# Kernel optimization log

Hardware: AMD Instinct MI355X
Metric: run time of the kernel (lower is better)

Reference implementation:

```python
import jax, jax.numpy as jnp
import numpy as np

B, T, D, K = 16, 8192, 64, 1024


def setup_inputs() -> dict:
    key = jax.random.key(0)
    k1, k2 = jax.random.split(key)
    x = jax.random.normal(k1, (B, T, D, 1), dtype=jnp.float32)
    weight = jax.random.normal(k2, (K, D), dtype=jnp.float32)
    return {"x": x, "weight": weight}


def reference(x, weight):
    # x: [B, T, D, 1] -> squeeze trailing dim -> [B, T, D]
    xs = jnp.squeeze(x, axis=-1)
    x2 = jnp.sum(xs * xs, axis=-1, keepdims=True)          # [B, T, 1]
    e2 = jnp.sum(weight * weight, axis=-1)                 # [K]
    xe = jnp.einsum('btd,kd->btk', xs, weight)             # [B, T, K]
    dist2 = x2 - 2.0 * xe + e2                             # [B, T, K]
    indices = jnp.argmin(dist2, axis=-1)                   # [B, T] int
    quantized = jnp.take(weight, indices, axis=0)          # [B, T, D]
    return quantized, indices
```

## Files before the change

### kernel.cpp

```cpp
#include <hip/hip_runtime.h>

#define MTOK  131072
#define DIMD  64
#define KCODE 1024
#define TPB   128

typedef __bf16 bf16x8 __attribute__((ext_vector_type(8)));
typedef float  f32x4  __attribute__((ext_vector_type(4)));

__device__ __forceinline__ f32x4 mfma16(bf16x8 a, bf16x8 b, f32x4 c) {
    return __builtin_amdgcn_mfma_f32_16x16x32_bf16(a, b, c, 0, 0, 0);
}

__global__ __launch_bounds__(256) void prep_kernel(
    const float* __restrict__ w, __bf16* __restrict__ wpk,
    float* __restrict__ e2n, float* __restrict__ e2) {
    int cb  = blockIdx.x;
    int tid = threadIdx.x;
    int win = tid >> 6, lane = tid & 63;
    int q = lane >> 4, m = lane & 15;
    int k = cb * 16 + m;
    int d0 = (win & 1) * 32 + q * 8;
    const float* src = w + (size_t)k * DIMD + d0;
    float4 v0 = *(const float4*)(src);
    float4 v1 = *(const float4*)(src + 4);
    float f[8] = {v0.x, v0.y, v0.z, v0.w, v1.x, v1.y, v1.z, v1.w};
    bf16x8 o;
#pragma unroll
    for (int j = 0; j < 8; ++j) {
        __bf16 h = (__bf16)f[j];
        o[j] = (win < 2) ? h : (__bf16)(f[j] - (float)h);
    }
    *(bf16x8*)(wpk + ((size_t)(cb * 4 + win) * 64 + lane) * 8) = o;

    if (tid < 16) {
        int k2 = cb * 16 + tid;
        const float4* row = (const float4*)(w + (size_t)k2 * DIMD);
        float s = 0.f;
#pragma unroll
        for (int i = 0; i < 16; ++i) {
            float4 v = row[i];
            s = fmaf(v.x, v.x, s); s = fmaf(v.y, v.y, s);
            s = fmaf(v.z, v.z, s); s = fmaf(v.w, v.w, s);
        }
        e2[k2]  = s;
        e2n[k2] = -0.5f * s;
    }
}

__global__ __launch_bounds__(256, 4) void vq_main(
    const float* __restrict__ x, const float* __restrict__ wfull,
    const __bf16* __restrict__ wpk, const float* __restrict__ e2n_g,
    const float* __restrict__ e2_g, float* __restrict__ out) {

    const int tid  = threadIdx.x;
    const int blk  = blockIdx.x;
    const int lane = tid & 63;
    const int wv   = tid >> 6;
    const int q    = lane >> 4;
    const int m    = lane & 15;
    const size_t tok0 = (size_t)blk * TPB + wv * 32;

    bf16x8 bx[2][4];
#pragma unroll
    for (int tg = 0; tg < 2; ++tg) {
        const float* xr = x + (tok0 + tg * 16 + m) * DIMD;
#pragma unroll
        for (int h = 0; h < 2; ++h) {
            float4 v0 = *(const float4*)(xr + h * 32 + q * 8);
            float4 v1 = *(const float4*)(xr + h * 32 + q * 8 + 4);
            float f[8] = {v0.x, v0.y, v0.z, v0.w, v1.x, v1.y, v1.z, v1.w};
            bf16x8 hi, lo;
#pragma unroll
            for (int j = 0; j < 8; ++j) {
                __bf16 hh = (__bf16)f[j];
                hi[j] = hh;
                lo[j] = (__bf16)(f[j] - (float)hh);
            }
            bx[tg][h]     = hi;
            bx[tg][2 + h] = lo;
        }
    }

    float b1[2], b2[2]; int i1[2];
#pragma unroll
    for (int tg = 0; tg < 2; ++tg) { b1[tg] = -3e38f; b2[tg] = -3e38f; i1[tg] = 0; }

    auto step = [&](bf16x8 f0, bf16x8 f1, bf16x8 f2, bf16x8 f3, f32x4 ee, int cbase) {
#pragma unroll
        for (int tg = 0; tg < 2; ++tg) {
            f32x4 t = mfma16(f0, bx[tg][0], ee);
            t = mfma16(f1, bx[tg][1], t);
            t = mfma16(f0, bx[tg][2], t);
            t = mfma16(f1, bx[tg][3], t);
            t = mfma16(f2, bx[tg][0], t);
            t = mfma16(f3, bx[tg][1], t);
#pragma unroll
            for (int r = 0; r < 4; ++r) {
                float a   = t[r];
                int idxv  = cbase + q * 4 + r;
                bool gt   = a > b1[tg];
                i1[tg] = gt ? idxv : i1[tg];
                b2[tg] = __builtin_amdgcn_fmed3f(a, b1[tg], b2[tg]);
                b1[tg] = fmaxf(a, b1[tg]);
            }
        }
    };

    const __bf16* wb = wpk + lane * 8;
    const float*  eb = e2n_g + q * 4;
    bf16x8 A0 = *(const bf16x8*)(wb + 0);
    bf16x8 A1 = *(const bf16x8*)(wb + 512);
    bf16x8 A2 = *(const bf16x8*)(wb + 1024);
    bf16x8 A3 = *(const bf16x8*)(wb + 1536);
    f32x4  EA = *(const f32x4*)(eb);

    for (int cb = 0; cb < 64; cb += 2) {
        const __bf16* pB = wb + (size_t)(cb + 1) * 2048;
        bf16x8 B0 = *(const bf16x8*)(pB + 0);
        bf16x8 B1 = *(const bf16x8*)(pB + 512);
        bf16x8 B2 = *(const bf16x8*)(pB + 1024);
        bf16x8 B3 = *(const bf16x8*)(pB + 1536);
        f32x4  EB = *(const f32x4*)(eb + (cb + 1) * 16);

        step(A0, A1, A2, A3, EA, cb * 16);

        if (cb + 2 < 64) {
            const __bf16* pA = wb + (size_t)(cb + 2) * 2048;
            A0 = *(const bf16x8*)(pA + 0);
            A1 = *(const bf16x8*)(pA + 512);
            A2 = *(const bf16x8*)(pA + 1024);
            A3 = *(const bf16x8*)(pA + 1536);
            EA = *(const f32x4*)(eb + (cb + 2) * 16);
        }
        step(B0, B1, B2, B3, EB, (cb + 1) * 16);
    }

    float B1f[2], B2f[2]; int I1f[2];
#pragma unroll
    for (int tg = 0; tg < 2; ++tg) {
        float B1 = b1[tg], B2 = b2[tg]; int I1 = i1[tg];
#pragma unroll
        for (int mask = 16; mask <= 32; mask <<= 1) {
            float ob1 = __shfl_xor(B1, mask);
            float ob2 = __shfl_xor(B2, mask);
            int   oi  = __shfl_xor(I1, mask);
            bool take = (ob1 > B1) || (ob1 == B1 && oi < I1);
            B2 = fmaxf(fminf(ob1, B1), fmaxf(ob2, B2));
            I1 = take ? oi : I1;
            B1 = fmaxf(ob1, B1);
        }
        B1f[tg] = B1; B2f[tg] = B2; I1f[tg] = I1;
    }

    int myidx;
    {
        int src = lane & 15;
        int v0 = __shfl(I1f[0], src);
        int v1 = __shfl(I1f[1], src);
        myidx = ((lane >> 4) & 1) ? v1 : v0;
    }

#pragma unroll
    for (int tg = 0; tg < 2; ++tg) {
        unsigned long long msk =
            __ballot((lane < 16) && (B1f[tg] - B2f[tg] < 2e-3f));
        while (msk) {
            int mm = __ffsll((unsigned long long)msk) - 1;
            msk &= msk - 1;
            int tloc = tg * 16 + mm;
            const float4* xr = (const float4*)(x + (tok0 + tloc) * DIMD);
            float bv = 3e38f; int bi = 0;
            for (int j = 0; j < 16; ++j) {
                int k = lane * 16 + j;
                const float4* wr = (const float4*)(wfull + (size_t)k * DIMD);
                float s = 0.f;
#pragma unroll
                for (int i = 0; i < 16; ++i) {
                    float4 xv = xr[i], wv4 = wr[i];
                    s = fmaf(xv.x, wv4.x, s); s = fmaf(xv.y, wv4.y, s);
                    s = fmaf(xv.z, wv4.z, s); s = fmaf(xv.w, wv4.w, s);
                }
                float dv = fmaf(-2.f, s, e2_g[k]);
                if (dv < bv) { bv = dv; bi = k; }
            }
#pragma unroll
            for (int mask2 = 1; mask2 <= 32; mask2 <<= 1) {
                float ov = __shfl_xor(bv, mask2);
                int   oi = __shfl_xor(bi, mask2);
                bool take = (ov < bv) || (ov == bv && oi < bi);
                bv = take ? ov : bv;
                bi = take ? oi : bi;
            }
            myidx = (lane == tloc) ? bi : myidx;
        }
    }

    if (lane < 32)
        out[(size_t)MTOK * DIMD + tok0 + lane] = (float)myidx;

    {
        float* obase = out + tok0 * DIMD;
#pragma unroll
        for (int j = 0; j < 8; ++j) {
            int srcl = j * 4 + (lane >> 4);
            int gi   = __shfl(myidx, srcl);
            float4 v = *(const float4*)(wfull + (size_t)gi * DIMD + (lane & 15) * 4);
            *(float4*)(obase + j * 256 + lane * 4) = v;
        }
    }
}

extern "C" void kernel_launch(void* const* d_in, const int* in_sizes, int n_in,
                              void* d_out, int out_size, void* d_ws, size_t ws_size,
                              hipStream_t stream) {
    const float* x = (const float*)d_in[0];
    const float* w = (const float*)d_in[1];
    float* out = (float*)d_out;

    __bf16* wpk = (__bf16*)d_ws;
    float*  e2n = (float*)((char*)d_ws + 262144);
    float*  e2  = (float*)((char*)d_ws + 266240);

    prep_kernel<<<64, 256, 0, stream>>>(w, wpk, e2n, e2);
    vq_main<<<MTOK / TPB, 256, 0, stream>>>(x, w, wpk, e2n, e2, out);
}
```

Before: 152.1 us.

## Deepen codebook prefetch to four stages and split norm computation into extra blocks

The main loop now keeps four codebook tiles in flight in registers instead of two, issuing the load for tile cb+4 before computing tile cb, so global-load latency is hidden further ahead. The prep kernel moves the per-code squared-norm computation into four extra blocks of 256 threads, so the 64 packing blocks no longer have 16 threads doing serial norm loops. Holding more prefetched tiles raises register pressure and could push vq_main below its occupancy target of 4 blocks or cause spills.

```diff
diff --git a/kernel.cpp b/kernel.cpp
--- a/kernel.cpp
+++ b/kernel.cpp
@@ -15,26 +15,27 @@
 __global__ __launch_bounds__(256) void prep_kernel(
     const float* __restrict__ w, __bf16* __restrict__ wpk,
     float* __restrict__ e2n, float* __restrict__ e2) {
-    int cb  = blockIdx.x;
+    int b   = blockIdx.x;
     int tid = threadIdx.x;
-    int win = tid >> 6, lane = tid & 63;
-    int q = lane >> 4, m = lane & 15;
-    int k = cb * 16 + m;
-    int d0 = (win & 1) * 32 + q * 8;
-    const float* src = w + (size_t)k * DIMD + d0;
-    float4 v0 = *(const float4*)(src);
-    float4 v1 = *(const float4*)(src + 4);
-    float f[8] = {v0.x, v0.y, v0.z, v0.w, v1.x, v1.y, v1.z, v1.w};
-    bf16x8 o;
-#pragma unroll
-    for (int j = 0; j < 8; ++j) {
-        __bf16 h = (__bf16)f[j];
-        o[j] = (win < 2) ? h : (__bf16)(f[j] - (float)h);
-    }
-    *(bf16x8*)(wpk + ((size_t)(cb * 4 + win) * 64 + lane) * 8) = o;
-
-    if (tid < 16) {
-        int k2 = cb * 16 + tid;
+    if (b < 64) {
+        int cb  = b;
+        int win = tid >> 6, lane = tid & 63;
+        int q = lane >> 4, m = lane & 15;
+        int k = cb * 16 + m;
+        int d0 = (win & 1) * 32 + q * 8;
+        const float* src = w + (size_t)k * DIMD + d0;
+        float4 v0 = *(const float4*)(src);
+        float4 v1 = *(const float4*)(src + 4);
+        float f[8] = {v0.x, v0.y, v0.z, v0.w, v1.x, v1.y, v1.z, v1.w};
+        bf16x8 o;
+#pragma unroll
+        for (int j = 0; j < 8; ++j) {
+            __bf16 h = (__bf16)f[j];
+            o[j] = (win < 2) ? h : (__bf16)(f[j] - (float)h);
+        }
+        *(bf16x8*)(wpk + ((size_t)(cb * 4 + win) * 64 + lane) * 8) = o;
+    } else {
+        int k2 = (b - 64) * 256 + tid;
         const float4* row = (const float4*)(w + (size_t)k2 * DIMD);
         float s = 0.f;
 #pragma unroll
@@ -109,31 +110,33 @@
 
     const __bf16* wb = wpk + lane * 8;
     const float*  eb = e2n_g + q * 4;
-    bf16x8 A0 = *(const bf16x8*)(wb + 0);
-    bf16x8 A1 = *(const bf16x8*)(wb + 512);
-    bf16x8 A2 = *(const bf16x8*)(wb + 1024);
-    bf16x8 A3 = *(const bf16x8*)(wb + 1536);
-    f32x4  EA = *(const f32x4*)(eb);
-
-    for (int cb = 0; cb < 64; cb += 2) {
-        const __bf16* pB = wb + (size_t)(cb + 1) * 2048;
-        bf16x8 B0 = *(const bf16x8*)(pB + 0);
-        bf16x8 B1 = *(const bf16x8*)(pB + 512);
-        bf16x8 B2 = *(const bf16x8*)(pB + 1024);
-        bf16x8 B3 = *(const bf16x8*)(pB + 1536);
-        f32x4  EB = *(const f32x4*)(eb + (cb + 1) * 16);
-
-        step(A0, A1, A2, A3, EA, cb * 16);
-
-        if (cb + 2 < 64) {
-            const __bf16* pA = wb + (size_t)(cb + 2) * 2048;
-            A0 = *(const bf16x8*)(pA + 0);
-            A1 = *(const bf16x8*)(pA + 512);
-            A2 = *(const bf16x8*)(pA + 1024);
-            A3 = *(const bf16x8*)(pA + 1536);
-            EA = *(const f32x4*)(eb + (cb + 2) * 16);
-        }
-        step(B0, B1, B2, B3, EB, (cb + 1) * 16);
+    bf16x8 F0[4], F1[4], F2[4], F3[4];
+    f32x4  E[4];
+#pragma unroll
+    for (int p = 0; p < 4; ++p) {
+        const __bf16* pp = wb + (size_t)p * 2048;
+        F0[p] = *(const bf16x8*)(pp + 0);
+        F1[p] = *(const bf16x8*)(pp + 512);
+        F2[p] = *(const bf16x8*)(pp + 1024);
+        F3[p] = *(const bf16x8*)(pp + 1536);
+        E[p]  = *(const f32x4*)(eb + p * 16);
+    }
+    for (int cb = 0; cb < 64; cb += 4) {
+#pragma unroll
+        for (int p = 0; p < 4; ++p) {
+            bf16x8 a0 = F0[p], a1 = F1[p], a2 = F2[p], a3 = F3[p];
+            f32x4  ee = E[p];
+            int nx = cb + 4 + p;
+            if (nx < 64) {
+                const __bf16* pp = wb + (size_t)nx * 2048;
+                F0[p] = *(const bf16x8*)(pp + 0);
+                F1[p] = *(const bf16x8*)(pp + 512);
+                F2[p] = *(const bf16x8*)(pp + 1024);
+                F3[p] = *(const bf16x8*)(pp + 1536);
+                E[p]  = *(const f32x4*)(eb + nx * 16);
+            }
+            step(a0, a1, a2, a3, ee, (cb + p) * 16);
+        }
     }
 
     float B1f[2], B2f[2]; int I1f[2];
@@ -222,6 +225,6 @@
     float*  e2n = (float*)((char*)d_ws + 262144);
     float*  e2  = (float*)((char*)d_ws + 266240);
 
-    prep_kernel<<<64, 256, 0, stream>>>(w, wpk, e2n, e2);
+    prep_kernel<<<68, 256, 0, stream>>>(w, wpk, e2n, e2);
     vq_main<<<MTOK / TPB, 256, 0, stream>>>(x, w, wpk, e2n, e2, out);
 }
```

After: 426.8 us. 2.81x slower.
